# Performance work log

Measured on AMD Instinct MI355X. Metric: run time of the kernel, lower is better.

Reference implementation:

```python
import jax, jax.numpy as jnp
import numpy as np

EMBED = 2048
HEADS = 16
HEAD_DIM = EMBED // HEADS


def setup_inputs() -> dict:
    key = jax.random.key(0)
    ks = jax.random.split(key, 9)
    s = 1.0 / np.sqrt(EMBED)
    inp = {"x": jax.random.normal(ks[0], (2, 2048, EMBED), dtype=jnp.float32)}
    for i, name in enumerate(["q", "k", "v", "o"]):
        inp[f"W{name}"] = jax.random.uniform(ks[1 + 2 * i], (EMBED, EMBED), dtype=jnp.float32, minval=-s, maxval=s)
        inp[f"b{name}"] = jax.random.uniform(ks[2 + 2 * i], (EMBED,), dtype=jnp.float32, minval=-s, maxval=s)
    return inp


def reference(x, Wq, bq, Wk, bk, Wv, bv, Wo, bo):
    B, S, E = x.shape
    def split_heads(t):
        return t.reshape(B, S, HEADS, HEAD_DIM).transpose(0, 2, 1, 3)  # [B,H,S,D]
    q = split_heads(x @ Wq.T + bq)
    k = split_heads(x @ Wk.T + bk)
    v = split_heads(x @ Wv.T + bv)
    scale = 1.0 / np.sqrt(HEAD_DIM)
    scores = jnp.einsum("bhqd,bhkd->bhqk", q, k) * scale  # [B,H,S,S]
    causal = jnp.tril(jnp.ones((S, S), dtype=bool))
    scores = jnp.where(causal[None, None], scores, -jnp.inf)
    attn = jax.nn.softmax(scores, axis=-1)
    out = jnp.einsum("bhqk,bhkd->bhqd", attn, v)  # [B,H,S,D]
    out = out.transpose(0, 2, 1, 3).reshape(B, S, E)
    return out @ Wo.T + bo
```

## Files before the change

kernel.cpp:

```cpp
#include <hip/hip_runtime.h>

typedef unsigned short u16;
typedef unsigned int u32;
typedef __attribute__((ext_vector_type(8))) short bf16x8;
typedef __attribute__((ext_vector_type(4))) float f32x4;

#define MFMA(a, b, c) __builtin_amdgcn_mfma_f32_16x16x32_bf16((a), (b), (c), 0, 0, 0)

__device__ inline u16 f2bf(float f) {
  u32 u = __float_as_uint(f);
  u = (u + 0x7fffu + ((u >> 16) & 1u)) >> 16;
  return (u16)u;
}

__device__ inline void gld16(u16* lds, const u16* g) {
  __builtin_amdgcn_global_load_lds((const __attribute__((address_space(1))) void*)g,
                                   (__attribute__((address_space(3))) void*)lds,
                                   16, 0, 0);
}

__global__ __launch_bounds__(256) void cvt_all(const float* __restrict__ x,
                                               const float* __restrict__ wa,
                                               const float* __restrict__ wb,
                                               const float* __restrict__ wc,
                                               const float* __restrict__ wd,
                                               uint2* __restrict__ dst) {
  int i = blockIdx.x * 256 + threadIdx.x;
  const float* s;
  int off;
  if (i < 2097152) {
    s = x; off = i;
  } else {
    int j = i - 2097152;
    int which = j >> 20;
    off = j & 1048575;
    s = (which == 0) ? wa : (which == 1) ? wb : (which == 2) ? wc : wd;
  }
  float4 f = ((const float4*)s)[off];
  u32 lo = (u32)f2bf(f.x) | ((u32)f2bf(f.y) << 16);
  u32 hi = (u32)f2bf(f.z) | ((u32)f2bf(f.w) << 16);
  dst[i] = make_uint2(lo, hi);
}

__device__ inline void gemm_core(const u16* __restrict__ A, const u16* __restrict__ W,
                                 u16* As, u16* Bs, int m0, int n0, f32x4 acc[4][4]) {
  const int K = 2048;
  const int NT = 64;
  int t = threadIdx.x, w = t >> 6, l = t & 63;
  int wr = (w >> 1) * 64, wc = (w & 1) * 64;
  int fr = l & 15, fg = l >> 4;
  int r0 = t >> 2;
  int r1 = 64 + r0;
  int c00 = (t & 3) ^ ((r0 >> 1) & 3);
  int c01 = (t & 3) ^ ((r1 >> 1) & 3);
  const u16* gA = A + (size_t)m0 * K;
  const u16* gB = W + (size_t)n0 * K;
  size_t a0 = (size_t)r0 * K + c00 * 8;
  size_t a1 = (size_t)r1 * K + c01 * 8;
#pragma unroll
  for (int p = 0; p < 2; ++p) {
    u16* sa = As + p * 4096;
    u16* sb = Bs + p * 4096;
    int kk = p * 32;
    gld16(sa + w * 512, gA + a0 + kk);
    gld16(sa + 2048 + w * 512, gA + a1 + kk);
    gld16(sb + w * 512, gB + a0 + kk);
    gld16(sb + 2048 + w * 512, gB + a1 + kk);
  }
  for (int kt = 0; kt < NT; ++kt) {
    int kt2 = (kt + 2 < NT) ? (kt + 2) : (NT - 1);
    u16* sa = As + ((kt + 2) & 3) * 4096;
    u16* sb = Bs + ((kt + 2) & 3) * 4096;
    int kk = kt2 * 32;
    gld16(sa + w * 512, gA + a0 + kk);
    gld16(sa + 2048 + w * 512, gA + a1 + kk);
    gld16(sb + w * 512, gB + a0 + kk);
    gld16(sb + 2048 + w * 512, gB + a1 + kk);
    asm volatile("s_waitcnt vmcnt(8)\n\ts_barrier" ::: "memory");
    const u16* ca = As + (kt & 3) * 4096;
    const u16* cb = Bs + (kt & 3) * 4096;
    bf16x8 af[4], bfv[4];
#pragma unroll
    for (int i = 0; i < 4; ++i) {
      int ar = wr + i * 16 + fr;
      af[i] = *(const bf16x8*)&ca[ar * 32 + ((fg ^ ((ar >> 1) & 3)) << 3)];
    }
#pragma unroll
    for (int i = 0; i < 4; ++i) {
      int br = wc + i * 16 + fr;
      bfv[i] = *(const bf16x8*)&cb[br * 32 + ((fg ^ ((br >> 1) & 3)) << 3)];
    }
    __builtin_amdgcn_s_setprio(1);
#pragma unroll
    for (int mi = 0; mi < 4; ++mi)
#pragma unroll
      for (int ni = 0; ni < 4; ++ni)
        acc[mi][ni] = MFMA(af[mi], bfv[ni], acc[mi][ni]);
    __builtin_amdgcn_s_setprio(0);
  }
}

__global__ __launch_bounds__(512, 2) void qkv_gemm(
    const u16* __restrict__ X, const u16* __restrict__ Wq, const u16* __restrict__ Wk,
    const u16* __restrict__ Wv, const float* __restrict__ bq, const float* __restrict__ bk,
    const float* __restrict__ bv, u16* __restrict__ Qo, u16* __restrict__ Ko,
    u16* __restrict__ Vo) {
  __shared__ __attribute__((aligned(16))) u16 As[32768];
  __shared__ __attribute__((aligned(16))) u16 Bs[32768];
  const int K = 2048, NT = 64;
  int which = blockIdx.x >> 3;
  int n0 = (blockIdx.x & 7) * 256;
  int m0 = blockIdx.y * 256;
  const u16* W = (which == 0) ? Wq : (which == 1) ? Wk : Wv;
  const float* bias = (which == 0) ? bq : (which == 1) ? bk : bv;
  u16* out = (which == 0) ? Qo : (which == 1) ? Ko : Vo;
  float scale = (which == 0) ? 0.08838834764831845f : 1.0f;
  int t = threadIdx.x, w = t >> 6, l = t & 63;
  int wm = w >> 2, wn = w & 3;
  int fr = l & 15, fg = l >> 4;
  int r0 = t >> 2;
  int c0 = (t & 3) ^ ((r0 >> 1) & 3);
  const u16* gA = X + (size_t)m0 * K;
  const u16* gB = W + (size_t)n0 * K;
  size_t a0 = (size_t)r0 * K + c0 * 8;
  size_t a1 = a0 + (size_t)128 * K;
  f32x4 zero4 = {0.f, 0.f, 0.f, 0.f};
  f32x4 acc[8][4];
#pragma unroll
  for (int i = 0; i < 8; ++i)
#pragma unroll
    for (int j = 0; j < 4; ++j) acc[i][j] = zero4;
#pragma unroll
  for (int p = 0; p < 2; ++p) {
    u16* sa = As + p * 8192;
    u16* sb = Bs + p * 8192;
    int kk = p * 32;
    gld16(sa + w * 512, gA + a0 + kk);
    gld16(sa + 4096 + w * 512, gA + a1 + kk);
    gld16(sb + w * 512, gB + a0 + kk);
    gld16(sb + 4096 + w * 512, gB + a1 + kk);
  }
  for (int kt = 0; kt < NT; ++kt) {
    int kt2 = (kt + 2 < NT) ? (kt + 2) : (NT - 1);
    u16* sa = As + ((kt + 2) & 3) * 8192;
    u16* sb = Bs + ((kt + 2) & 3) * 8192;
    int kk = kt2 * 32;
    gld16(sa + w * 512, gA + a0 + kk);
    gld16(sa + 4096 + w * 512, gA + a1 + kk);
    gld16(sb + w * 512, gB + a0 + kk);
    gld16(sb + 4096 + w * 512, gB + a1 + kk);
    asm volatile("s_waitcnt vmcnt(8)\n\ts_barrier" ::: "memory");
    const u16* ca = As + (kt & 3) * 8192;
    const u16* cb = Bs + (kt & 3) * 8192;
    bf16x8 af[8], bfv[4];
#pragma unroll
    for (int i = 0; i < 8; ++i) {
      int ar = wm * 128 + i * 16 + fr;
      af[i] = *(const bf16x8*)&ca[ar * 32 + ((fg ^ ((ar >> 1) & 3)) << 3)];
    }
#pragma unroll
    for (int i = 0; i < 4; ++i) {
      int br = wn * 64 + i * 16 + fr;
      bfv[i] = *(const bf16x8*)&cb[br * 32 + ((fg ^ ((br >> 1) & 3)) << 3)];
    }
    __builtin_amdgcn_s_setprio(1);
#pragma unroll
    for (int mi = 0; mi < 8; ++mi)
#pragma unroll
      for (int ni = 0; ni < 4; ++ni)
        acc[mi][ni] = MFMA(af[mi], bfv[ni], acc[mi][ni]);
    __builtin_amdgcn_s_setprio(0);
  }
  if (which == 2) {
#pragma unroll
    for (int mi = 0; mi < 8; ++mi) {
#pragma unroll
      for (int ni = 0; ni < 4; ++ni) {
        int row = m0 + wm * 128 + mi * 16 + (l >> 4) * 4;
        int col = n0 + wn * 64 + ni * 16 + (l & 15);
        float bb = bias[col];
        int h = col >> 7, d = col & 127;
        int b = row >> 11, s = row & 2047;
        u32 p0 = (u32)f2bf(acc[mi][ni][0] + bb) | ((u32)f2bf(acc[mi][ni][1] + bb) << 16);
        u32 p1 = (u32)f2bf(acc[mi][ni][2] + bb) | ((u32)f2bf(acc[mi][ni][3] + bb) << 16);
        *(uint2*)&out[((size_t)(b * 16 + h) * 128 + d) * 2048 + s] = make_uint2(p0, p1);
      }
    }
  } else {
#pragma unroll
    for (int mi = 0; mi < 8; ++mi) {
#pragma unroll
      for (int ni = 0; ni < 4; ++ni) {
        int row = m0 + wm * 128 + mi * 16 + (l >> 4) * 4;
        int col = n0 + wn * 64 + ni * 16 + (l & 15);
        float bb = bias[col];
        int h = col >> 7, d = col & 127;
#pragma unroll
        for (int i = 0; i < 4; ++i) {
          int m = row + i;
          int b = m >> 11, s = m & 2047;
          float v = (acc[mi][ni][i] + bb) * scale;
          out[(((size_t)b * 16 + h) * 2048 + s) * 128 + d] = f2bf(v);
        }
      }
    }
  }
}

__global__ __launch_bounds__(256, 2) void oproj_gemm(const u16* __restrict__ A,
                                                     const u16* __restrict__ W,
                                                     const float* __restrict__ bias,
                                                     float* __restrict__ out) {
  __shared__ __attribute__((aligned(16))) u16 As[16384];
  __shared__ __attribute__((aligned(16))) u16 Bs[16384];
  int n0 = blockIdx.x * 128, m0 = blockIdx.y * 128;
  f32x4 zero4 = {0.f, 0.f, 0.f, 0.f};
  f32x4 acc[4][4];
#pragma unroll
  for (int i = 0; i < 4; ++i)
#pragma unroll
    for (int j = 0; j < 4; ++j) acc[i][j] = zero4;
  gemm_core(A, W, As, Bs, m0, n0, acc);
  int t = threadIdx.x, w = t >> 6, l = t & 63;
  int wr = (w >> 1) * 64, wc = (w & 1) * 64;
#pragma unroll
  for (int mi = 0; mi < 4; ++mi) {
#pragma unroll
    for (int ni = 0; ni < 4; ++ni) {
      int row = m0 + wr + mi * 16 + (l >> 4) * 4;
      int col = n0 + wc + ni * 16 + (l & 15);
      float bb = bias[col];
#pragma unroll
      for (int i = 0; i < 4; ++i) out[(size_t)(row + i) * 2048 + col] = acc[mi][ni][i] + bb;
    }
  }
}

__global__ __launch_bounds__(256, 2) void attn_fwd(const u16* __restrict__ Q,
                                                   const u16* __restrict__ K,
                                                   const u16* __restrict__ Vt,
                                                   u16* __restrict__ AO) {
  __shared__ __attribute__((aligned(16))) u16 Ks[8192];
  __shared__ __attribute__((aligned(16))) u16 Vts[8192];
  __shared__ __attribute__((aligned(16))) u16 Pl[8192];
  const int D = 128;
  int b3 = blockIdx.x;
  int bh = b3 & 31;
  int xq = b3 >> 5;
  int qt = (xq < 8) ? (15 - xq) : (xq - 8);
  int t = threadIdx.x, w = t >> 6, l = t & 63, g = l >> 4, c = l & 15;
  size_t base = (size_t)bh * 2048 * 128;
  const u16* Vbh = Vt + base;
  int q0 = qt * 128;
  int qrw = q0 + w * 32;
  bf16x8 qf[2][4];
#pragma unroll
  for (int mi = 0; mi < 2; ++mi) {
    const u16* qp = Q + base + (size_t)(qrw + mi * 16 + c) * D + g * 8;
#pragma unroll
    for (int ks = 0; ks < 4; ++ks) qf[mi][ks] = *(const bf16x8*)(qp + ks * 32);
  }
  f32x4 zero4 = {0.f, 0.f, 0.f, 0.f};
  f32x4 oacc[2][8];
#pragma unroll
  for (int mi = 0; mi < 2; ++mi)
#pragma unroll
    for (int i = 0; i < 8; ++i) oacc[mi][i] = zero4;
  float mrow[2][4], lrow[2][4];
#pragma unroll
  for (int mi = 0; mi < 2; ++mi)
#pragma unroll
    for (int i = 0; i < 4; ++i) { mrow[mi][i] = -1e30f; lrow[mi][i] = 0.f; }
  char* pw = (char*)(Pl + w * 2048);
  int ktmax = 2 * qt + 1;
  for (int kt = 0; kt <= ktmax; ++kt) {
    int kv0 = kt * 64;
    __syncthreads();
#pragma unroll
    for (int ci = 0; ci < 4; ++ci) {
      int row = w * 16 + ci * 4 + g;
      int cc = c ^ (row & 7);
      gld16(Ks + w * 2048 + ci * 512, K + base + (size_t)(kv0 + row) * D + cc * 8);
    }
#pragma unroll
    for (int ci = 0; ci < 4; ++ci) {
      int vr = ci * 32 + w * 8 + (l >> 3);
      int vslot = (l & 7) ^ ((l >> 3) & 7);
      gld16(Vts + ci * 2048 + w * 512, Vbh + (size_t)vr * 2048 + kv0 + vslot * 8);
    }
    __syncthreads();
    if (kv0 <= qrw + 31) {
      f32x4 sacc[2][4];
#pragma unroll
      for (int mi = 0; mi < 2; ++mi)
#pragma unroll
        for (int n = 0; n < 4; ++n) sacc[mi][n] = zero4;
#pragma unroll
      for (int ks = 0; ks < 4; ++ks) {
#pragma unroll
        for (int n = 0; n < 4; ++n) {
          int row = n * 16 + c;
          bf16x8 kf = *(const bf16x8*)&Ks[row * 128 + (((ks * 4 + g) ^ (c & 7)) << 3)];
          sacc[0][n] = MFMA(qf[0][ks], kf, sacc[0][n]);
          sacc[1][n] = MFMA(qf[1][ks], kf, sacc[1][n]);
        }
      }
      float sc[2][4][4];
#pragma unroll
      for (int mi = 0; mi < 2; ++mi)
#pragma unroll
        for (int n = 0; n < 4; ++n)
#pragma unroll
          for (int i = 0; i < 4; ++i) sc[mi][n][i] = sacc[mi][n][i];
      if (kv0 + 63 > qrw) {
#pragma unroll
        for (int mi = 0; mi < 2; ++mi)
#pragma unroll
          for (int n = 0; n < 4; ++n) {
            int kv = kv0 + n * 16 + c;
#pragma unroll
            for (int i = 0; i < 4; ++i)
              if (kv > qrw + mi * 16 + g * 4 + i) sc[mi][n][i] = -1e30f;
          }
      }
      float tmax[2][4];
#pragma unroll
      for (int mi = 0; mi < 2; ++mi)
#pragma unroll
        for (int i = 0; i < 4; ++i)
          tmax[mi][i] = fmaxf(fmaxf(sc[mi][0][i], sc[mi][1][i]), fmaxf(sc[mi][2][i], sc[mi][3][i]));
#pragma unroll
      for (int x = 1; x < 16; x <<= 1)
#pragma unroll
        for (int mi = 0; mi < 2; ++mi)
#pragma unroll
          for (int i = 0; i < 4; ++i) tmax[mi][i] = fmaxf(tmax[mi][i], __shfl_xor(tmax[mi][i], x));
      float corr[2][4], rs[2][4];
#pragma unroll
      for (int mi = 0; mi < 2; ++mi)
#pragma unroll
        for (int i = 0; i < 4; ++i) {
          float mn = fmaxf(mrow[mi][i], tmax[mi][i]);
          corr[mi][i] = __expf(mrow[mi][i] - mn);
          mrow[mi][i] = mn;
          rs[mi][i] = 0.f;
        }
      float ps[2][4][4];
#pragma unroll
      for (int mi = 0; mi < 2; ++mi)
#pragma unroll
        for (int n = 0; n < 4; ++n)
#pragma unroll
          for (int i = 0; i < 4; ++i) {
            ps[mi][n][i] = __expf(sc[mi][n][i] - mrow[mi][i]);
            rs[mi][i] += ps[mi][n][i];
          }
#pragma unroll
      for (int x = 1; x < 16; x <<= 1)
#pragma unroll
        for (int mi = 0; mi < 2; ++mi)
#pragma unroll
          for (int i = 0; i < 4; ++i) rs[mi][i] += __shfl_xor(rs[mi][i], x);
#pragma unroll
      for (int mi = 0; mi < 2; ++mi)
#pragma unroll
        for (int i = 0; i < 4; ++i) lrow[mi][i] = lrow[mi][i] * corr[mi][i] + rs[mi][i];
#pragma unroll
      for (int mi = 0; mi < 2; ++mi)
#pragma unroll
        for (int nf = 0; nf < 8; ++nf)
#pragma unroll
          for (int i = 0; i < 4; ++i) oacc[mi][nf][i] *= corr[mi][i];
#pragma unroll
      for (int mi = 0; mi < 2; ++mi)
#pragma unroll
        for (int n = 0; n < 4; ++n)
#pragma unroll
          for (int i = 0; i < 4; ++i) {
            int row = mi * 16 + g * 4 + i;
            *(u16*)(pw + row * 128 + ((n * 32 + c * 2) ^ ((row & 7) << 4))) = f2bf(ps[mi][n][i]);
          }
#pragma unroll
      for (int ks = 0; ks < 2; ++ks) {
        bf16x8 pf0 = *(const bf16x8*)(pw + (c)*128 + ((ks * 64 + g * 16) ^ ((c & 7) << 4)));
        bf16x8 pf1 = *(const bf16x8*)(pw + (16 + c) * 128 + ((ks * 64 + g * 16) ^ ((c & 7) << 4)));
#pragma unroll
        for (int nf = 0; nf < 8; ++nf) {
          bf16x8 vf = *(const bf16x8*)&Vts[(nf * 16 + c) * 64 + (((ks * 4 + g) ^ (c & 7)) << 3)];
          oacc[0][nf] = MFMA(pf0, vf, oacc[0][nf]);
          oacc[1][nf] = MFMA(pf1, vf, oacc[1][nf]);
        }
      }
    }
  }
  int b = bh >> 4, h = bh & 15;
#pragma unroll
  for (int mi = 0; mi < 2; ++mi)
#pragma unroll
    for (int nf = 0; nf < 8; ++nf) {
      int d = h * 128 + nf * 16 + c;
#pragma unroll
      for (int i = 0; i < 4; ++i) {
        int q = qrw + mi * 16 + g * 4 + i;
        AO[((size_t)b * 2048 + q) * 2048 + d] = f2bf(oacc[mi][nf][i] / lrow[mi][i]);
      }
    }
}

extern "C" void kernel_launch(void* const* d_in, const int* in_sizes, int n_in,
                              void* d_out, int out_size, void* d_ws, size_t ws_size,
                              hipStream_t stream) {
  const float* x = (const float*)d_in[0];
  const float* Wq = (const float*)d_in[1];
  const float* bq = (const float*)d_in[2];
  const float* Wk = (const float*)d_in[3];
  const float* bk = (const float*)d_in[4];
  const float* Wv = (const float*)d_in[5];
  const float* bv = (const float*)d_in[6];
  const float* Wo = (const float*)d_in[7];
  const float* bo = (const float*)d_in[8];
  float* out = (float*)d_out;

  u16* xb = (u16*)d_ws;
  u16* Wqb = xb + 8388608;
  u16* Wkb = Wqb + 4194304;
  u16* Wvb = Wkb + 4194304;
  u16* Wob = Wvb + 4194304;
  u16* Qb = Wob + 4194304;
  u16* Kb = Qb + 8388608;
  u16* Vb = Kb + 8388608;
  u16* AOb = xb;

  cvt_all<<<24576, 256, 0, stream>>>(x, Wq, Wk, Wv, Wo, (uint2*)d_ws);
  qkv_gemm<<<dim3(24, 16), 512, 0, stream>>>(xb, Wqb, Wkb, Wvb, bq, bk, bv, Qb, Kb, Vb);
  attn_fwd<<<512, 256, 0, stream>>>(Qb, Kb, Vb, AOb);
  oproj_gemm<<<dim3(16, 32), 256, 0, stream>>>(AOb, Wob, bo, out);
}
```

Baseline: 286.6 us.

## Double-buffer K/V tiles in attention with async prefetch of next tile

Doubles the K and V LDS buffers and issues the global-to-LDS loads for the next key tile before computing on the current one. A manual s_waitcnt vmcnt(8) plus barrier waits only for the current tile's loads, and a trailing barrier guards buffer reuse. The aim is to hide global load latency behind the MFMA work. LDS use grows from 48KB to 80KB per block, which may drop occupancy below the two blocks per CU the launch bounds request. The last iteration redundantly reloads the final tile.

```diff
diff --git a/kernel.cpp b/kernel.cpp
--- a/kernel.cpp
+++ b/kernel.cpp
@@ -240,8 +240,8 @@
                                                    const u16* __restrict__ K,
                                                    const u16* __restrict__ Vt,
                                                    u16* __restrict__ AO) {
-  __shared__ __attribute__((aligned(16))) u16 Ks[8192];
-  __shared__ __attribute__((aligned(16))) u16 Vts[8192];
+  __shared__ __attribute__((aligned(16))) u16 Ks[16384];
+  __shared__ __attribute__((aligned(16))) u16 Vts[16384];
   __shared__ __attribute__((aligned(16))) u16 Pl[8192];
   const int D = 128;
   int b3 = blockIdx.x;
@@ -253,6 +253,8 @@
   const u16* Vbh = Vt + base;
   int q0 = qt * 128;
   int qrw = q0 + w * 32;
+  int krow = w * 16 + (l >> 2) % 4 * 4 + g;
+  (void)krow;
   bf16x8 qf[2][4];
 #pragma unroll
   for (int mi = 0; mi < 2; ++mi) {
@@ -273,22 +275,29 @@
     for (int i = 0; i < 4; ++i) { mrow[mi][i] = -1e30f; lrow[mi][i] = 0.f; }
   char* pw = (char*)(Pl + w * 2048);
   int ktmax = 2 * qt + 1;
+#define STAGE_TILE(BUF, KV0)                                                          \
+  {                                                                                   \
+    _Pragma("unroll") for (int ci = 0; ci < 4; ++ci) {                                \
+      int row = w * 16 + ci * 4 + g;                                                  \
+      int cc = c ^ (row & 7);                                                         \
+      gld16(Ks + (BUF)*8192 + w * 2048 + ci * 512,                                    \
+            K + base + (size_t)((KV0) + row) * D + cc * 8);                           \
+    }                                                                                 \
+    _Pragma("unroll") for (int ci = 0; ci < 4; ++ci) {                                \
+      int vr = ci * 32 + w * 8 + (l >> 3);                                            \
+      int vslot = (l & 7) ^ ((l >> 3) & 7);                                           \
+      gld16(Vts + (BUF)*8192 + ci * 2048 + w * 512,                                   \
+            Vbh + (size_t)vr * 2048 + (KV0) + vslot * 8);                             \
+    }                                                                                 \
+  }
+  STAGE_TILE(0, 0)
   for (int kt = 0; kt <= ktmax; ++kt) {
     int kv0 = kt * 64;
-    __syncthreads();
-#pragma unroll
-    for (int ci = 0; ci < 4; ++ci) {
-      int row = w * 16 + ci * 4 + g;
-      int cc = c ^ (row & 7);
-      gld16(Ks + w * 2048 + ci * 512, K + base + (size_t)(kv0 + row) * D + cc * 8);
-    }
-#pragma unroll
-    for (int ci = 0; ci < 4; ++ci) {
-      int vr = ci * 32 + w * 8 + (l >> 3);
-      int vslot = (l & 7) ^ ((l >> 3) & 7);
-      gld16(Vts + ci * 2048 + w * 512, Vbh + (size_t)vr * 2048 + kv0 + vslot * 8);
-    }
-    __syncthreads();
+    int ktn = (kt + 1 <= ktmax) ? (kt + 1) : ktmax;
+    STAGE_TILE((kt + 1) & 1, ktn * 64)
+    asm volatile("s_waitcnt vmcnt(8)\n\ts_barrier" ::: "memory");
+    const u16* Kb = Ks + (kt & 1) * 8192;
+    const u16* Vb2 = Vts + (kt & 1) * 8192;
     if (kv0 <= qrw + 31) {
       f32x4 sacc[2][4];
 #pragma unroll
@@ -300,7 +309,7 @@
 #pragma unroll
         for (int n = 0; n < 4; ++n) {
           int row = n * 16 + c;
-          bf16x8 kf = *(const bf16x8*)&Ks[row * 128 + (((ks * 4 + g) ^ (c & 7)) << 3)];
+          bf16x8 kf = *(const bf16x8*)&Kb[row * 128 + (((ks * 4 + g) ^ (c & 7)) << 3)];
           sacc[0][n] = MFMA(qf[0][ks], kf, sacc[0][n]);
           sacc[1][n] = MFMA(qf[1][ks], kf, sacc[1][n]);
         }
@@ -386,12 +395,13 @@
         bf16x8 pf1 = *(const bf16x8*)(pw + (16 + c) * 128 + ((ks * 64 + g * 16) ^ ((c & 7) << 4)));
 #pragma unroll
         for (int nf = 0; nf < 8; ++nf) {
-          bf16x8 vf = *(const bf16x8*)&Vts[(nf * 16 + c) * 64 + (((ks * 4 + g) ^ (c & 7)) << 3)];
+          bf16x8 vf = *(const bf16x8*)&Vb2[(nf * 16 + c) * 64 + (((ks * 4 + g) ^ (c & 7)) << 3)];
           oacc[0][nf] = MFMA(pf0, vf, oacc[0][nf]);
           oacc[1][nf] = MFMA(pf1, vf, oacc[1][nf]);
         }
       }
     }
+    __syncthreads();
   }
   int b = bh >> 4, h = bh & 15;
 #pragma unroll
```

Result: no change. 286.3 us (-0.1%).
